# Kernel tuning notes

Hardware: AMD Instinct MI355X
Metric: run time of the kernel (lower is better)

## Reference

```python
import jax, jax.numpy as jnp
import numpy as np

B, T, D = 2, 2048, 1024
K, F = 8, 4096
LAMBDA = 0.5


def setup_inputs() -> dict:
    key = jax.random.key(0)
    ks = jax.random.split(key, 8)
    s = 0.02
    return {
        "x": jax.random.normal(ks[0], (B, T, D), dtype=jnp.float32),
        "prev_logits": jax.random.normal(ks[1], (B, T, K), dtype=jnp.float32),
        "Wt": jax.random.normal(ks[2], (D, K), dtype=jnp.float32) * s,
        "Wgt": jax.random.normal(ks[3], (K, K), dtype=jnp.float32) * s,
        "We_logits": jnp.zeros((K,), dtype=jnp.float32),
        "W1": jax.random.normal(ks[4], (K, D, F), dtype=jnp.float32) * s,
        "b1": jnp.zeros((K, F), dtype=jnp.float32),
        "W2": jax.random.normal(ks[5], (K, F, D), dtype=jnp.float32) * s,
        "b2": jnp.zeros((K, D), dtype=jnp.float32),
    }


def reference(x, prev_logits, Wt, Wgt, We_logits, W1, b1, W2, b2):
    # gating: softmax over router logits, sigmoid-threshold multi-hot mask
    logits = jnp.einsum("btd,dk->btk", x, Wt) + jnp.einsum("btk,kj->btj", prev_logits, Wgt)
    st = jax.nn.softmax(logits, axis=-1)                       # (B,T,K)
    We = jax.nn.sigmoid(We_logits)                             # (K,)
    mask = (st > LAMBDA * We).astype(x.dtype)                  # (B,T,K)
    g = st * mask
    sel_counts = mask.sum(axis=(0, 1))                         # (K,)
    avg_density = mask.sum(axis=-1).mean()                     # scalar

    # dense multi-expert FFN: every expert on every token (dropout=0 / eval)
    h = jax.nn.gelu(jnp.einsum("btd,kdf->bktf", x, W1) + b1[:, None, :], approximate=False)
    outk = jnp.einsum("bktf,kfd->bktd", h, W2) + b2[:, None, :]  # (B,K,T,D)
    y = jnp.einsum("btk,bktd->btd", g, outk)
    y = y / (g.sum(axis=-1, keepdims=True) + 1e-6)
    return y, jax.lax.stop_gradient(logits), sel_counts, avg_density
```

## Files before the change

### kernel.cpp

```cpp
#include <hip/hip_runtime.h>
#include <cstdint>
#include <cstddef>

#define NB 2
#define NTT 2048
#define ND 1024
#define NK 8
#define NF 4096
#define NTOK (NB*NTT)
#define LAMBDA_C 0.5f

#define Y_SZ   (NTOK*ND)
#define LG_OFF Y_SZ
#define SC_OFF (LG_OFF + NTOK*NK)
#define AD_OFF (SC_OFF + NK)

#define WS_CNT    0
#define WS_SEG    8
#define WS_NTILES 17
#define WS_TILEK  32
#define WS_TILER  1056
#define WS_PTOK   4096
#define WS_PCOEF  36864
#define WS_COEF   69632
#define WS_X16    102400
#define WS_H      2199552

#define BM 128
#define BN 64
#define BK 64
#define SPLITK2 4
#define KT 16

#define AOFF0 0u
#define AOFF1 16384u
#define BOFF0 32768u
#define BOFF1 40960u

typedef float  f32x4 __attribute__((ext_vector_type(4)));
typedef _Float16 f16x8 __attribute__((ext_vector_type(8)));
typedef unsigned int u32x2 __attribute__((ext_vector_type(2)));
typedef unsigned int u32x4 __attribute__((ext_vector_type(4)));

__device__ __forceinline__ unsigned int pkrtz(float a, float b){
    auto h = __builtin_amdgcn_cvt_pkrtz(a, b);
    return __builtin_bit_cast(unsigned int, h);
}
__device__ __forceinline__ float gelu_exact(float v){
    return 0.5f * v * (1.0f + erff(v * 0.70710678118654752440f));
}

__global__ __launch_bounds__(256) void k_xcast(const float* __restrict__ x,
                                               unsigned short* __restrict__ x16)
{
    int i = (blockIdx.x*256 + threadIdx.x) * 16;
    const f32x4* src = (const f32x4*)(x + i);
    f32x4 v0 = src[0], v1 = src[1], v2 = src[2], v3 = src[3];
    u32x4 o0 = {pkrtz(v0[0],v0[1]), pkrtz(v0[2],v0[3]), pkrtz(v1[0],v1[1]), pkrtz(v1[2],v1[3])};
    u32x4 o1 = {pkrtz(v2[0],v2[1]), pkrtz(v2[2],v2[3]), pkrtz(v3[0],v3[1]), pkrtz(v3[2],v3[3])};
    *(u32x4*)(x16 + i)     = o0;
    *(u32x4*)(x16 + i + 8) = o1;
}

__global__ __launch_bounds__(256) void k_gating(
    const float* __restrict__ x, const float* __restrict__ pl,
    const float* __restrict__ Wt, const float* __restrict__ Wgt,
    const float* __restrict__ Wel, float* __restrict__ out,
    float* __restrict__ coef, int* __restrict__ cnt)
{
    int t = blockIdx.x;
    const float* xt = x + (size_t)t * ND;
    float acc[NK] = {0,0,0,0,0,0,0,0};
    for (int d = threadIdx.x; d < ND; d += 256){
        float xv = xt[d];
        const float4* w = (const float4*)(Wt + (size_t)d * NK);
        float4 w0 = w[0], w1 = w[1];
        acc[0] += xv*w0.x; acc[1] += xv*w0.y; acc[2] += xv*w0.z; acc[3] += xv*w0.w;
        acc[4] += xv*w1.x; acc[5] += xv*w1.y; acc[6] += xv*w1.z; acc[7] += xv*w1.w;
    }
    __shared__ float red[4][NK];
    #pragma unroll
    for (int k = 0; k < NK; k++){
        float v = acc[k];
        #pragma unroll
        for (int off = 32; off; off >>= 1) v += __shfl_down(v, off);
        if ((threadIdx.x & 63) == 0) red[threadIdx.x >> 6][k] = v;
    }
    __syncthreads();
    if (threadIdx.x == 0){
        const float* p = pl + (size_t)t * NK;
        float pv[NK];
        #pragma unroll
        for (int j = 0; j < NK; j++) pv[j] = p[j];
        float lg[NK]; float mx = -1e30f;
        #pragma unroll
        for (int k = 0; k < NK; k++){
            float v = red[0][k] + red[1][k] + red[2][k] + red[3][k];
            #pragma unroll
            for (int j = 0; j < NK; j++) v += pv[j] * Wgt[j*NK + k];
            lg[k] = v; mx = fmaxf(mx, v);
            out[LG_OFF + (size_t)t*NK + k] = v;
        }
        float e[NK]; float s = 0.f;
        #pragma unroll
        for (int k = 0; k < NK; k++){ e[k] = expf(lg[k] - mx); s += e[k]; }
        float g[NK]; float gsum = 0.f;
        #pragma unroll
        for (int k = 0; k < NK; k++){
            float st = e[k] / s;
            float we = 1.f / (1.f + expf(-Wel[k]));
            bool m = st > LAMBDA_C * we;
            g[k] = m ? st : 0.f;
            gsum += g[k];
        }
        float inv = 1.f / (gsum + 1e-6f);
        #pragma unroll
        for (int k = 0; k < NK; k++){
            coef[(size_t)t*NK + k] = g[k] * inv;
            if (g[k] > 0.f) atomicAdd(&cnt[k], 1);
        }
    }
}

__global__ __launch_bounds__(256) void k_scan(
    const float* __restrict__ coef, int* __restrict__ wsi,
    float* __restrict__ wsf, int pair_cap)
{
    int k = blockIdx.x;
    const int* cnt = wsi + WS_CNT;
    int base = 0;
    for (int j = 0; j < k; j++) base += cnt[j];
    int tid = threadIdx.x, lane = tid & 63, w = tid >> 6;
    __shared__ int wsum[4];
    __shared__ int sbase;
    if (tid == 0){
        sbase = base;
        wsi[WS_SEG + k] = base;
        if (k == NK-1) wsi[WS_SEG + NK] = base + cnt[k];
    }
    __syncthreads();
    int* ptok = wsi + WS_PTOK;
    float* pc = wsf + WS_PCOEF;
    for (int c0 = 0; c0 < NTOK; c0 += 256){
        int t = c0 + tid;
        float c = coef[(size_t)t*NK + k];
        bool m = c > 0.f;
        unsigned long long bal = __ballot(m);
        int pre = __popcll(bal & ((1ull << lane) - 1ull));
        if (lane == 0) wsum[w] = __popcll(bal);
        __syncthreads();
        int b = sbase;
        for (int j = 0; j < w; j++) b += wsum[j];
        if (m){
            int pos = b + pre;
            if (pos < pair_cap){ ptok[pos] = t; pc[pos] = c; }
        }
        __syncthreads();
        if (tid == 0) sbase += wsum[0] + wsum[1] + wsum[2] + wsum[3];
        __syncthreads();
    }
}

__global__ void k_tiles(int* __restrict__ wsi, float* __restrict__ out, int pair_cap)
{
    if (threadIdx.x == 0 && blockIdx.x == 0){
        const int* cnt = wsi + WS_CNT;
        const int* seg = wsi + WS_SEG;
        int total = 0;
        for (int k = 0; k < NK; k++){ total += cnt[k]; out[SC_OFF + k] = (float)cnt[k]; }
        out[AD_OFF] = (float)total / (float)NTOK;
        int nt = 0;
        for (int k = 0; k < NK; k++){
            int e = min(seg[k+1], pair_cap);
            for (int r = seg[k]; r < e; r += BM){
                wsi[WS_TILEK + nt] = k; wsi[WS_TILER + nt] = r; nt++;
            }
        }
        wsi[WS_NTILES] = nt;
    }
}

#define XCD_PART_LOOP(nwork)                                              \
    int q_ = (nwork) >> 3, rr_ = (nwork) & 7;                             \
    int xcd_ = blockIdx.x & 7;                                            \
    int slot_ = blockIdx.x >> 3;                                          \
    int nslot_ = gridDim.x >> 3;                                          \
    int cntw_ = q_ + (xcd_ < rr_ ? 1 : 0);                                \
    int start_ = xcd_ * q_ + (xcd_ < rr_ ? xcd_ : rr_);                   \
    for (int p_ = slot_; p_ < cntw_; p_ += nslot_)


#define LOAD_A(dst_, tt_)                                                 \
    { const unsigned short* an_ = asrc + (tt_)*BK;                        \
      _Pragma("unroll")                                                   \
      for (int j_ = 0; j_ < 4; j_++) dst_[j_] = *(const u32x4*)(an_ + j_*8); }

#define LOAD_B(dst_, tt_, LDW_)                                           \
    { const float* bn_ = bsrc + (size_t)((tt_)*BK + bkq*4)*LDW_;          \
      _Pragma("unroll")                                                   \
      for (int r_ = 0; r_ < 4; r_++) dst_[r_] = *(const f32x4*)(bn_ + (size_t)r_*LDW_); }

#define STAGE_A(src_, AO_)                                                \
    { _Pragma("unroll")                                                   \
      for (int j_ = 0; j_ < 4; j_++){                                     \
          unsigned off_ = (AO_) + (unsigned)arow*128u +                   \
              ((((unsigned)(ahalf*4 + j_)) ^ (unsigned)(arow & 7)) << 4); \
          *(u32x4*)(&lds[off_]) = src_[j_];                               \
      } }

#define STAGE_B(src_, BO_)                                                \
    { unsigned wA_[4], wB_[4];                                            \
      _Pragma("unroll")                                                   \
      for (int r_ = 0; r_ < 4; r_++){                                     \
          wA_[r_] = pkrtz(src_[r_][0], src_[r_][1]);                      \
          wB_[r_] = pkrtz(src_[r_][2], src_[r_][3]);                      \
      }                                                                   \
      _Pragma("unroll")                                                   \
      for (int j_ = 0; j_ < 4; j_++){                                     \
          unsigned s0_ = (j_ < 2) ? wA_[1] : wB_[1];                      \
          unsigned s1_ = (j_ < 2) ? wA_[0] : wB_[0];                      \
          unsigned s2_ = (j_ < 2) ? wA_[3] : wB_[3];                      \
          unsigned s3_ = (j_ < 2) ? wA_[2] : wB_[2];                      \
          unsigned sel_ = (j_ & 1) ? 0x07060302u : 0x05040100u;           \
          unsigned o0_ = __builtin_amdgcn_perm(s0_, s1_, sel_);           \
          unsigned o1_ = __builtin_amdgcn_perm(s2_, s3_, sel_);           \
          unsigned col_ = (unsigned)(bcc*4 + j_);                         \
          unsigned off_ = (BO_) + col_*128u +                             \
              (((unsigned)(bkq*8)) ^ ((col_ & 7u) << 4));                 \
          *(u32x2*)(&lds[off_]) = (u32x2){o0_, o1_};                      \
      } }

#define MFMA_RD(AO_, BO_)                                                 \
    { _Pragma("unroll")                                                   \
      for (int kk_ = 0; kk_ < 2; kk_++){                                  \
          unsigned sb_ = ((unsigned)(kk_*64 + q*16)) ^ swzL;              \
          f16x8 af_[4], bf_[2];                                           \
          _Pragma("unroll")                                               \
          for (int m_ = 0; m_ < 4; m_++)                                  \
              af_[m_] = *(const f16x8*)(&lds[(AO_) + (unsigned)(wr*64 + m_*16 + l15)*128u + sb_]); \
          _Pragma("unroll")                                               \
          for (int n_ = 0; n_ < 2; n_++)                                  \
              bf_[n_] = *(const f16x8*)(&lds[(BO_) + (unsigned)(wc*32 + n_*16 + l15)*128u + sb_]); \
          _Pragma("unroll")                                               \
          for (int m_ = 0; m_ < 4; m_++)                                  \
          _Pragma("unroll")                                               \
          for (int n_ = 0; n_ < 2; n_++)                                  \
              acc[m_][n_] = __builtin_amdgcn_mfma_f32_16x16x32_f16(af_[m_], bf_[n_], acc[m_][n_], 0, 0, 0); \
      } }

#define STEP_SYNC()                                                       \
    asm volatile("s_waitcnt lgkmcnt(0)" ::: "memory");                    \
    __builtin_amdgcn_s_barrier();                                         \
    __builtin_amdgcn_sched_barrier(0);

__global__ __launch_bounds__(256, 3) void k_gemm1(
    const unsigned short* __restrict__ x16, const float* __restrict__ W1,
    const float* __restrict__ b1, const int* __restrict__ wsi,
    unsigned short* __restrict__ hbuf, int pair_cap)
{
    __shared__ char lds[49152];
    __shared__ int stok[BM];
    const int* seg  = wsi + WS_SEG;
    const int* tk   = wsi + WS_TILEK;
    const int* tr   = wsi + WS_TILER;
    const int* ptok = wsi + WS_PTOK;
    int ntm = wsi[WS_NTILES];
    int nwork = ntm * (NF / BN);
    int tid  = threadIdx.x;
    int lane = tid & 63;
    int w    = tid >> 6;
    int wr = w >> 1, wc = w & 1;
    int l15 = lane & 15, q = lane >> 4;
    unsigned swzL = (unsigned)((l15 & 7) << 4);
    int arow = tid >> 1, ahalf = tid & 1;
    int bkq = tid >> 4, bcc = tid & 15;

    XCD_PART_LOOP(nwork){
        int widx = start_ + p_;
        int mt = widx % ntm;
        int ft = widx / ntm;
        int kexp = tk[mt];
        int row0 = tr[mt];
        int nrows = min(BM, seg[kexp+1] - row0);
        int f0 = ft * BN;
        __syncthreads();
        if (tid < BM){
            int r = row0 + tid;
            stok[tid] = (tid < nrows && r < pair_cap) ? ptok[r] : ptok[row0];
        }
        __syncthreads();
        const unsigned short* asrc = x16 + (size_t)stok[arow]*ND + ahalf*32;
        const float* bsrc = W1 + (size_t)kexp*ND*NF + f0 + bcc*4;
        u32x4 ga0[4], ga1[4]; f32x4 gb0[4], gb1[4];
        LOAD_A(ga0, 0) LOAD_B(gb0, 0, NF)
        LOAD_A(ga1, 1) LOAD_B(gb1, 1, NF)
        f32x4 acc[4][2] = {};
        for (int t = 0; t < KT; t += 2){
            STAGE_A(ga0, AOFF0) STAGE_B(gb0, BOFF0)
            if (t + 2 < KT){ LOAD_A(ga0, t+2) LOAD_B(gb0, t+2, NF) }
            STEP_SYNC()
            MFMA_RD(AOFF0, BOFF0)
            STAGE_A(ga1, AOFF1) STAGE_B(gb1, BOFF1)
            if (t + 3 < KT){ LOAD_A(ga1, t+3) LOAD_B(gb1, t+3, NF) }
            STEP_SYNC()
            MFMA_RD(AOFF1, BOFF1)
        }
        const float* b1k = b1 + (size_t)kexp*NF;
        #pragma unroll
        for (int n = 0; n < 2; n++){
            int f = f0 + wc*32 + n*16 + l15;
            float bv = b1k[f];
            #pragma unroll
            for (int m = 0; m < 4; m++){
                int rl = wr*64 + m*16 + q*4;
                #pragma unroll
                for (int i = 0; i < 4; i++){
                    int r = rl + i;
                    if (r < nrows && row0 + r < pair_cap){
                        float v = gelu_exact(acc[m][n][i] + bv);
                        hbuf[(size_t)(row0+r)*NF + f] = (unsigned short)(pkrtz(v, 0.f) & 0xffffu);
                    }
                }
            }
        }
    }
}

__global__ __launch_bounds__(256, 3) void k_gemm2(
    const unsigned short* __restrict__ hbuf, const float* __restrict__ W2,
    const float* __restrict__ b2, const int* __restrict__ wsi,
    const float* __restrict__ wsf, float* __restrict__ out, int pair_cap)
{
    __shared__ char lds[49152];
    __shared__ int stok[BM];
    __shared__ float scoef[BM];
    const int* seg  = wsi + WS_SEG;
    const int* tk   = wsi + WS_TILEK;
    const int* tr   = wsi + WS_TILER;
    const int* ptok = wsi + WS_PTOK;
    const float* pcoef = wsf + WS_PCOEF;
    int ntm = wsi[WS_NTILES];
    int nwork = ntm * (ND / BN) * SPLITK2;
    int tid  = threadIdx.x;
    int lane = tid & 63;
    int w    = tid >> 6;
    int wr = w >> 1, wc = w & 1;
    int l15 = lane & 15, q = lane >> 4;
    unsigned swzL = (unsigned)((l15 & 7) << 4);
    int arow = tid >> 1, ahalf = tid & 1;
    int bkq = tid >> 4, bcc = tid & 15;

    XCD_PART_LOOP(nwork){
        int widx = start_ + p_;
        int mt = widx % ntm;
        int rest = widx / ntm;
        int dt = rest & 15;
        int sp = rest >> 4;
        int kexp = tk[mt];
        int row0 = tr[mt];
        int nrows = min(BM, seg[kexp+1] - row0);
        int d0 = dt * BN;
        __syncthreads();
        if (tid < BM){
            int r = row0 + tid;
            bool v = (tid < nrows && r < pair_cap);
            stok[tid]  = v ? ptok[r] : 0;
            scoef[tid] = v ? pcoef[r] : 0.f;
        }
        __syncthreads();
        int hr = row0 + arow; if (hr >= pair_cap) hr = pair_cap - 1;
        const unsigned short* asrc = hbuf + (size_t)hr*NF + sp*(NF/SPLITK2) + ahalf*32;
        const float* bsrc = W2 + (size_t)kexp*NF*ND + (size_t)sp*(NF/SPLITK2)*ND + d0 + bcc*4;
        u32x4 ga0[4], ga1[4]; f32x4 gb0[4], gb1[4];
        LOAD_A(ga0, 0) LOAD_B(gb0, 0, ND)
        LOAD_A(ga1, 1) LOAD_B(gb1, 1, ND)
        f32x4 acc[4][2] = {};
        for (int t = 0; t < KT; t += 2){
            STAGE_A(ga0, AOFF0) STAGE_B(gb0, BOFF0)
            if (t + 2 < KT){ LOAD_A(ga0, t+2) LOAD_B(gb0, t+2, ND) }
            STEP_SYNC()
            MFMA_RD(AOFF0, BOFF0)
            STAGE_A(ga1, AOFF1) STAGE_B(gb1, BOFF1)
            if (t + 3 < KT){ LOAD_A(ga1, t+3) LOAD_B(gb1, t+3, ND) }
            STEP_SYNC()
            MFMA_RD(AOFF1, BOFF1)
        }
        const float* b2k = b2 + (size_t)kexp*ND;
        #pragma unroll
        for (int n = 0; n < 2; n++){
            int d = d0 + wc*32 + n*16 + l15;
            float bv = (sp == 0) ? b2k[d] : 0.f;
            #pragma unroll
            for (int m = 0; m < 4; m++){
                int rl = wr*64 + m*16 + q*4;
                #pragma unroll
                for (int i = 0; i < 4; i++){
                    int r = rl + i;
                    if (r < nrows && row0 + r < pair_cap){
                        float c = scoef[r];
                        atomicAdd(&out[(size_t)stok[r]*ND + d], c * (acc[m][n][i] + bv));
                    }
                }
            }
        }
    }
}

extern "C" void kernel_launch(void* const* d_in, const int* in_sizes, int n_in,
                              void* d_out, int out_size, void* d_ws, size_t ws_size,
                              hipStream_t stream)
{
    const float* x   = (const float*)d_in[0];
    const float* pl  = (const float*)d_in[1];
    const float* Wt  = (const float*)d_in[2];
    const float* Wgt = (const float*)d_in[3];
    const float* Wel = (const float*)d_in[4];
    const float* W1  = (const float*)d_in[5];
    const float* b1  = (const float*)d_in[6];
    const float* W2  = (const float*)d_in[7];
    const float* b2  = (const float*)d_in[8];
    float* out = (float*)d_out;
    int* wsi   = (int*)d_ws;
    float* wsf = (float*)d_ws;
    unsigned short* x16  = (unsigned short*)((char*)d_ws + (size_t)WS_X16*4);
    unsigned short* hbuf = (unsigned short*)((char*)d_ws + (size_t)WS_H*4);

    long long avail = (long long)ws_size - (long long)WS_H*4;
    long long cap = avail / ((long long)NF*2);
    if (cap > (long long)NTOK*NK) cap = (long long)NTOK*NK;
    if (cap < 0) cap = 0;
    int pair_cap = (int)cap;

    hipMemsetAsync(d_out, 0, (size_t)out_size*sizeof(float), stream);
    hipMemsetAsync(d_ws, 0, 32, stream);
    k_xcast<<<1024, 256, 0, stream>>>(x, x16);
    k_gating<<<NTOK, 256, 0, stream>>>(x, pl, Wt, Wgt, Wel, out, wsf + WS_COEF, wsi + WS_CNT);
    if (pair_cap > 0){
        k_scan<<<NK, 256, 0, stream>>>(wsf + WS_COEF, wsi, wsf, pair_cap);
        k_tiles<<<1, 64, 0, stream>>>(wsi, out, pair_cap);
        k_gemm1<<<2048, 256, 0, stream>>>(x16, W1, b1, wsi, hbuf, pair_cap);
        k_gemm2<<<2048, 256, 0, stream>>>(hbuf, W2, b2, wsi, wsf, out, pair_cap);
    }
}
```

Baseline: 244.7 us.

## Widen GEMM tiles to 128x128 with 32x32 MFMA and direct global-to-LDS A loads

```diff
diff --git a/kernel.cpp b/kernel.cpp
--- a/kernel.cpp
+++ b/kernel.cpp
@@ -27,19 +27,19 @@
 #define WS_H      2199552
 
 #define BM 128
-#define BN 64
+#define BN 128
 #define BK 64
 #define SPLITK2 4
 #define KT 16
 
-#define AOFF0 0u
-#define AOFF1 16384u
-#define BOFF0 32768u
-#define BOFF1 40960u
-
-typedef float  f32x4 __attribute__((ext_vector_type(4)));
+#define ASL0 0u
+#define ASL1 16384u
+#define BSL0 32768u
+#define BSL1 49152u
+
+typedef float  f32x4  __attribute__((ext_vector_type(4)));
+typedef float  f32x16 __attribute__((ext_vector_type(16)));
 typedef _Float16 f16x8 __attribute__((ext_vector_type(8)));
-typedef unsigned int u32x2 __attribute__((ext_vector_type(2)));
 typedef unsigned int u32x4 __attribute__((ext_vector_type(4)));
 
 __device__ __forceinline__ unsigned int pkrtz(float a, float b){
@@ -190,75 +190,86 @@
     for (int p_ = slot_; p_ < cntw_; p_ += nslot_)
 
 
-#define LOAD_A(dst_, tt_)                                                 \
-    { const unsigned short* an_ = asrc + (tt_)*BK;                        \
-      _Pragma("unroll")                                                   \
-      for (int j_ = 0; j_ < 4; j_++) dst_[j_] = *(const u32x4*)(an_ + j_*8); }
-
-#define LOAD_B(dst_, tt_, LDW_)                                           \
-    { const float* bn_ = bsrc + (size_t)((tt_)*BK + bkq*4)*LDW_;          \
-      _Pragma("unroll")                                                   \
-      for (int r_ = 0; r_ < 4; r_++) dst_[r_] = *(const f32x4*)(bn_ + (size_t)r_*LDW_); }
-
-#define STAGE_A(src_, AO_)                                                \
-    { _Pragma("unroll")                                                   \
-      for (int j_ = 0; j_ < 4; j_++){                                     \
-          unsigned off_ = (AO_) + (unsigned)arow*128u +                   \
-              ((((unsigned)(ahalf*4 + j_)) ^ (unsigned)(arow & 7)) << 4); \
-          *(u32x4*)(&lds[off_]) = src_[j_];                               \
-      } }
-
-#define STAGE_B(src_, BO_)                                                \
-    { unsigned wA_[4], wB_[4];                                            \
-      _Pragma("unroll")                                                   \
-      for (int r_ = 0; r_ < 4; r_++){                                     \
-          wA_[r_] = pkrtz(src_[r_][0], src_[r_][1]);                      \
-          wB_[r_] = pkrtz(src_[r_][2], src_[r_][3]);                      \
-      }                                                                   \
-      _Pragma("unroll")                                                   \
-      for (int j_ = 0; j_ < 4; j_++){                                     \
-          unsigned s0_ = (j_ < 2) ? wA_[1] : wB_[1];                      \
-          unsigned s1_ = (j_ < 2) ? wA_[0] : wB_[0];                      \
-          unsigned s2_ = (j_ < 2) ? wA_[3] : wB_[3];                      \
-          unsigned s3_ = (j_ < 2) ? wA_[2] : wB_[2];                      \
-          unsigned sel_ = (j_ & 1) ? 0x07060302u : 0x05040100u;           \
-          unsigned o0_ = __builtin_amdgcn_perm(s0_, s1_, sel_);           \
-          unsigned o1_ = __builtin_amdgcn_perm(s2_, s3_, sel_);           \
-          unsigned col_ = (unsigned)(bcc*4 + j_);                         \
-          unsigned off_ = (BO_) + col_*128u +                             \
-              (((unsigned)(bkq*8)) ^ ((col_ & 7u) << 4));                 \
-          *(u32x2*)(&lds[off_]) = (u32x2){o0_, o1_};                      \
-      } }
-
-#define MFMA_RD(AO_, BO_)                                                 \
-    { _Pragma("unroll")                                                   \
-      for (int kk_ = 0; kk_ < 2; kk_++){                                  \
-          unsigned sb_ = ((unsigned)(kk_*64 + q*16)) ^ swzL;              \
-          f16x8 af_[4], bf_[2];                                           \
-          _Pragma("unroll")                                               \
-          for (int m_ = 0; m_ < 4; m_++)                                  \
-              af_[m_] = *(const f16x8*)(&lds[(AO_) + (unsigned)(wr*64 + m_*16 + l15)*128u + sb_]); \
-          _Pragma("unroll")                                               \
-          for (int n_ = 0; n_ < 2; n_++)                                  \
-              bf_[n_] = *(const f16x8*)(&lds[(BO_) + (unsigned)(wc*32 + n_*16 + l15)*128u + sb_]); \
-          _Pragma("unroll")                                               \
-          for (int m_ = 0; m_ < 4; m_++)                                  \
-          _Pragma("unroll")                                               \
-          for (int n_ = 0; n_ < 2; n_++)                                  \
-              acc[m_][n_] = __builtin_amdgcn_mfma_f32_16x16x32_f16(af_[m_], bf_[n_], acc[m_][n_], 0, 0, 0); \
-      } }
-
-#define STEP_SYNC()                                                       \
-    asm volatile("s_waitcnt lgkmcnt(0)" ::: "memory");                    \
-    __builtin_amdgcn_s_barrier();                                         \
-    __builtin_amdgcn_sched_barrier(0);
-
-__global__ __launch_bounds__(256, 3) void k_gemm1(
+#define LOADB(tt_, LDW_)                                                  \
+  { const float* bn_ = bsrc + (size_t)((tt_)*BK + bu*8)*(LDW_);           \
+    _Pragma("unroll")                                                     \
+    for (int r9_ = 0; r9_ < 8; r9_++) gb[r9_] = *(const f32x4*)(bn_ + (size_t)r9_*(LDW_)); }
+
+#define CVTWRB(BO_)                                                       \
+  { _Pragma("unroll")                                                     \
+    for (int j9_ = 0; j9_ < 4; j9_++){                                    \
+        unsigned p0_ = pkrtz(gb[0][j9_], gb[1][j9_]);                     \
+        unsigned p1_ = pkrtz(gb[2][j9_], gb[3][j9_]);                     \
+        unsigned p2_ = pkrtz(gb[4][j9_], gb[5][j9_]);                     \
+        unsigned p3_ = pkrtz(gb[6][j9_], gb[7][j9_]);                     \
+        unsigned c9_ = (unsigned)(bg*4 + j9_);                            \
+        unsigned off9_ = (BO_) + c9_*128u + (((unsigned)bu*16u) ^ (((c9_>>1)&7u)<<4)); \
+        *(u32x4*)(&lds[off9_]) = (u32x4){p0_, p1_, p2_, p3_};             \
+    } }
+
+#define GLL_A(AO_, tt_)                                                   \
+  { _Pragma("unroll")                                                     \
+    for (int c9_ = 0; c9_ < 4; c9_++){                                    \
+        const unsigned short* g9_ = asrc[c9_] + (tt_)*BK + asw8;          \
+        __builtin_amdgcn_global_load_lds(                                 \
+            (const __attribute__((address_space(1))) void*)g9_,           \
+            (__attribute__((address_space(3))) void*)(&lds[(AO_) + (unsigned)((wv*4 + c9_)*1024)]), \
+            16, 0, 0);                                                    \
+    } }
+
+#define MFMA_PH(AO_, BO_)                                                 \
+  { __builtin_amdgcn_s_setprio(1);                                        \
+    _Pragma("unroll")                                                     \
+    for (int s9_ = 0; s9_ < 4; s9_++){                                    \
+        unsigned ko_ = (unsigned)(s9_*32) + ah16;                         \
+        f16x8 a0_ = *(const f16x8*)(&lds[(AO_) + arow0*128u + (ko_ ^ axr)]); \
+        f16x8 a1_ = *(const f16x8*)(&lds[(AO_) + arow1*128u + (ko_ ^ axr)]); \
+        f16x8 b0_ = *(const f16x8*)(&lds[(BO_) + bcol0*128u + (ko_ ^ bxr)]); \
+        f16x8 b1_ = *(const f16x8*)(&lds[(BO_) + bcol1*128u + (ko_ ^ bxr)]); \
+        acc00 = __builtin_amdgcn_mfma_f32_32x32x16_f16(a0_, b0_, acc00, 0,0,0); \
+        acc01 = __builtin_amdgcn_mfma_f32_32x32x16_f16(a0_, b1_, acc01, 0,0,0); \
+        acc10 = __builtin_amdgcn_mfma_f32_32x32x16_f16(a1_, b0_, acc10, 0,0,0); \
+        acc11 = __builtin_amdgcn_mfma_f32_32x32x16_f16(a1_, b1_, acc11, 0,0,0); \
+    }                                                                     \
+    __builtin_amdgcn_s_setprio(0); }
+
+#define PIPE_LOOP(LDW_)                                                   \
+    f32x16 acc00 = {0}, acc01 = {0}, acc10 = {0}, acc11 = {0};            \
+    LOADB(0, LDW_)                                                        \
+    GLL_A(ASL0, 0)                                                        \
+    for (int t = 0; t < KT-1; t++){                                       \
+        if ((t & 1) == 0){                                                \
+            CVTWRB(BSL0)                                                  \
+            LOADB(t+1, LDW_)                                              \
+            asm volatile("s_waitcnt vmcnt(8) lgkmcnt(0)" ::: "memory");   \
+            __builtin_amdgcn_s_barrier();                                 \
+            __builtin_amdgcn_sched_barrier(0);                            \
+            GLL_A(ASL1, t+1)                                              \
+            MFMA_PH(ASL0, BSL0)                                           \
+        } else {                                                          \
+            CVTWRB(BSL1)                                                  \
+            LOADB(t+1, LDW_)                                              \
+            asm volatile("s_waitcnt vmcnt(8) lgkmcnt(0)" ::: "memory");   \
+            __builtin_amdgcn_s_barrier();                                 \
+            __builtin_amdgcn_sched_barrier(0);                            \
+            GLL_A(ASL0, t+1)                                              \
+            MFMA_PH(ASL1, BSL1)                                           \
+        }                                                                 \
+    }                                                                     \
+    {                                     \
+        CVTWRB(BSL1)                                                      \
+        asm volatile("s_waitcnt vmcnt(0) lgkmcnt(0)" ::: "memory");       \
+        __builtin_amdgcn_s_barrier();                                     \
+        __builtin_amdgcn_sched_barrier(0);                                \
+        MFMA_PH(ASL1, BSL1)                                               \
+    }
+
+__global__ __launch_bounds__(256, 2) void k_gemm1(
     const unsigned short* __restrict__ x16, const float* __restrict__ W1,
     const float* __restrict__ b1, const int* __restrict__ wsi,
     unsigned short* __restrict__ hbuf, int pair_cap)
 {
-    __shared__ char lds[49152];
+    __shared__ char lds[65536];
     __shared__ int stok[BM];
     const int* seg  = wsi + WS_SEG;
     const int* tk   = wsi + WS_TILEK;
@@ -267,13 +278,20 @@
     int ntm = wsi[WS_NTILES];
     int nwork = ntm * (NF / BN);
     int tid  = threadIdx.x;
-    int lane = tid & 63;
-    int w    = tid >> 6;
-    int wr = w >> 1, wc = w & 1;
-    int l15 = lane & 15, q = lane >> 4;
-    unsigned swzL = (unsigned)((l15 & 7) << 4);
-    int arow = tid >> 1, ahalf = tid & 1;
-    int bkq = tid >> 4, bcc = tid & 15;
+    int L    = tid & 63;
+    int wv   = tid >> 6;
+    int wr = wv >> 1, wc = wv & 1;
+    int bu = tid >> 5, bg = tid & 31;
+    unsigned l31 = (unsigned)(L & 31);
+    unsigned arow0 = (unsigned)(wr*64) + l31;
+    unsigned arow1 = arow0 + 32u;
+    unsigned bcol0 = BSL0*0 + (unsigned)(wc*64) + l31;
+    unsigned bcol1 = bcol0 + 32u;
+    unsigned ah16 = (unsigned)((L >> 5) * 16);
+    unsigned axr  = (unsigned)((L & 7) << 4);
+    unsigned bxr  = ((l31 >> 1) & 7u) << 4;
+    int asw8 = ((L & 7) ^ (L >> 3)) * 8;
+    int srow = L >> 3;
 
     XCD_PART_LOOP(nwork){
         int widx = start_ + p_;
@@ -289,36 +307,28 @@
             stok[tid] = (tid < nrows && r < pair_cap) ? ptok[r] : ptok[row0];
         }
         __syncthreads();
-        const unsigned short* asrc = x16 + (size_t)stok[arow]*ND + ahalf*32;
-        const float* bsrc = W1 + (size_t)kexp*ND*NF + f0 + bcc*4;
-        u32x4 ga0[4], ga1[4]; f32x4 gb0[4], gb1[4];
-        LOAD_A(ga0, 0) LOAD_B(gb0, 0, NF)
-        LOAD_A(ga1, 1) LOAD_B(gb1, 1, NF)
-        f32x4 acc[4][2] = {};
-        for (int t = 0; t < KT; t += 2){
-            STAGE_A(ga0, AOFF0) STAGE_B(gb0, BOFF0)
-            if (t + 2 < KT){ LOAD_A(ga0, t+2) LOAD_B(gb0, t+2, NF) }
-            STEP_SYNC()
-            MFMA_RD(AOFF0, BOFF0)
-            STAGE_A(ga1, AOFF1) STAGE_B(gb1, BOFF1)
-            if (t + 3 < KT){ LOAD_A(ga1, t+3) LOAD_B(gb1, t+3, NF) }
-            STEP_SYNC()
-            MFMA_RD(AOFF1, BOFF1)
-        }
+        const unsigned short* asrc[4];
+        #pragma unroll
+        for (int c = 0; c < 4; c++)
+            asrc[c] = x16 + (size_t)stok[(wv*4 + c)*8 + srow] * ND;
+        const float* bsrc = W1 + (size_t)kexp*ND*NF + f0 + bg*4;
+        f32x4 gb[8];
+        PIPE_LOOP(NF)
         const float* b1k = b1 + (size_t)kexp*NF;
         #pragma unroll
         for (int n = 0; n < 2; n++){
-            int f = f0 + wc*32 + n*16 + l15;
+            int f = f0 + wc*64 + n*32 + (int)l31;
             float bv = b1k[f];
             #pragma unroll
-            for (int m = 0; m < 4; m++){
-                int rl = wr*64 + m*16 + q*4;
+            for (int m = 0; m < 2; m++){
+                int rbase = wr*64 + m*32 + 4*(L>>5);
+                const f32x16& a = (m==0) ? (n==0 ? acc00 : acc01) : (n==0 ? acc10 : acc11);
                 #pragma unroll
-                for (int i = 0; i < 4; i++){
-                    int r = rl + i;
-                    if (r < nrows && row0 + r < pair_cap){
-                        float v = gelu_exact(acc[m][n][i] + bv);
-                        hbuf[(size_t)(row0+r)*NF + f] = (unsigned short)(pkrtz(v, 0.f) & 0xffffu);
+                for (int rg = 0; rg < 16; rg++){
+                    int row = rbase + (rg&3) + 8*(rg>>2);
+                    if (row < nrows && row0 + row < pair_cap){
+                        float v = gelu_exact(a[rg] + bv);
+                        hbuf[(size_t)(row0+row)*NF + f] = (unsigned short)(pkrtz(v, 0.f) & 0xffffu);
                     }
                 }
             }
@@ -326,12 +336,12 @@
     }
 }
 
-__global__ __launch_bounds__(256, 3) void k_gemm2(
+__global__ __launch_bounds__(256, 2) void k_gemm2(
     const unsigned short* __restrict__ hbuf, const float* __restrict__ W2,
     const float* __restrict__ b2, const int* __restrict__ wsi,
     const float* __restrict__ wsf, float* __restrict__ out, int pair_cap)
 {
-    __shared__ char lds[49152];
+    __shared__ char lds[65536];
     __shared__ int stok[BM];
     __shared__ float scoef[BM];
     const int* seg  = wsi + WS_SEG;
@@ -342,20 +352,27 @@
     int ntm = wsi[WS_NTILES];
     int nwork = ntm * (ND / BN) * SPLITK2;
     int tid  = threadIdx.x;
-    int lane = tid & 63;
-    int w    = tid >> 6;
-    int wr = w >> 1, wc = w & 1;
-    int l15 = lane & 15, q = lane >> 4;
-    unsigned swzL = (unsigned)((l15 & 7) << 4);
-    int arow = tid >> 1, ahalf = tid & 1;
-    int bkq = tid >> 4, bcc = tid & 15;
+    int L    = tid & 63;
+    int wv   = tid >> 6;
+    int wr = wv >> 1, wc = wv & 1;
+    int bu = tid >> 5, bg = tid & 31;
+    unsigned l31 = (unsigned)(L & 31);
+    unsigned arow0 = (unsigned)(wr*64) + l31;
+    unsigned arow1 = arow0 + 32u;
+    unsigned bcol0 = (unsigned)(wc*64) + l31;
+    unsigned bcol1 = bcol0 + 32u;
+    unsigned ah16 = (unsigned)((L >> 5) * 16);
+    unsigned axr  = (unsigned)((L & 7) << 4);
+    unsigned bxr  = ((l31 >> 1) & 7u) << 4;
+    int asw8 = ((L & 7) ^ (L >> 3)) * 8;
+    int srow = L >> 3;
 
     XCD_PART_LOOP(nwork){
         int widx = start_ + p_;
         int mt = widx % ntm;
         int rest = widx / ntm;
-        int dt = rest & 15;
-        int sp = rest >> 4;
+        int dt = rest & 7;
+        int spk = rest >> 3;
         int kexp = tk[mt];
         int row0 = tr[mt];
         int nrows = min(BM, seg[kexp+1] - row0);
@@ -368,37 +385,31 @@
             scoef[tid] = v ? pcoef[r] : 0.f;
         }
         __syncthreads();
-        int hr = row0 + arow; if (hr >= pair_cap) hr = pair_cap - 1;
-        const unsigned short* asrc = hbuf + (size_t)hr*NF + sp*(NF/SPLITK2) + ahalf*32;
-        const float* bsrc = W2 + (size_t)kexp*NF*ND + (size_t)sp*(NF/SPLITK2)*ND + d0 + bcc*4;
-        u32x4 ga0[4], ga1[4]; f32x4 gb0[4], gb1[4];
-        LOAD_A(ga0, 0) LOAD_B(gb0, 0, ND)
-        LOAD_A(ga1, 1) LOAD_B(gb1, 1, ND)
-        f32x4 acc[4][2] = {};
-        for (int t = 0; t < KT; t += 2){
-            STAGE_A(ga0, AOFF0) STAGE_B(gb0, BOFF0)
-            if (t + 2 < KT){ LOAD_A(ga0, t+2) LOAD_B(gb0, t+2, ND) }
-            STEP_SYNC()
-            MFMA_RD(AOFF0, BOFF0)
-            STAGE_A(ga1, AOFF1) STAGE_B(gb1, BOFF1)
-            if (t + 3 < KT){ LOAD_A(ga1, t+3) LOAD_B(gb1, t+3, ND) }
-            STEP_SYNC()
-            MFMA_RD(AOFF1, BOFF1)
-        }
+        const unsigned short* asrc[4];
+        #pragma unroll
+        for (int c = 0; c < 4; c++){
+            int rg = row0 + (wv*4 + c)*8 + srow;
+            if (rg >= pair_cap) rg = pair_cap - 1;
+            asrc[c] = hbuf + (size_t)rg*NF + spk*(NF/SPLITK2);
+        }
+        const float* bsrc = W2 + (size_t)kexp*NF*ND + (size_t)spk*(NF/SPLITK2)*ND + d0 + bg*4;
+        f32x4 gb[8];
+        PIPE_LOOP(ND)
         const float* b2k = b2 + (size_t)kexp*ND;
         #pragma unroll
         for (int n = 0; n < 2; n++){
-            int d = d0 + wc*32 + n*16 + l15;
-            float bv = (sp == 0) ? b2k[d] : 0.f;
+            int d = d0 + wc*64 + n*32 + (int)l31;
+            float bv = (spk == 0) ? b2k[d] : 0.f;
             #pragma unroll
-            for (int m = 0; m < 4; m++){
-                int rl = wr*64 + m*16 + q*4;
+            for (int m = 0; m < 2; m++){
+                int rbase = wr*64 + m*32 + 4*(L>>5);
+                const f32x16& a = (m==0) ? (n==0 ? acc00 : acc01) : (n==0 ? acc10 : acc11);
                 #pragma unroll
-                for (int i = 0; i < 4; i++){
-                    int r = rl + i;
-                    if (r < nrows && row0 + r < pair_cap){
-                        float c = scoef[r];
-                        atomicAdd(&out[(size_t)stok[r]*ND + d], c * (acc[m][n][i] + bv));
+                for (int rg = 0; rg < 16; rg++){
+                    int row = rbase + (rg&3) + 8*(rg>>2);
+                    if (row < nrows && row0 + row < pair_cap){
+                        float c = scoef[row];
+                        atomicAdd(&out[(size_t)stok[row]*ND + d], c * (a[rg] + bv));
                     }
                 }
             }
```

Measured after the change: 262.5 us. 7.2% more time.
